# Kernel optimization log

Measured on AMD Instinct MI355X. Metric: run time of the kernel, lower is better.

## Reference

```python
import jax, jax.numpy as jnp
import numpy as np

KS = 5          # B-spline kernel_size per pseudo-coordinate dim
DIM = 2         # pseudo-coordinate dimensionality
NUM_GRAPHS = 64


def spline_conv(x, src, dst, edge_attr, W, root, bias):
    """Degree-1 open B-spline conv (torch-spline-conv semantics, aggr='mean').
    x: [N,Cin], edge_attr: [E,DIM] in [0,1], W: [KS**DIM,Cin,Cout]."""
    N = x.shape[0]
    E = src.shape[0]
    v = edge_attr * (KS - 1)                                   # [E,DIM]
    k_lo = jnp.clip(jnp.floor(v), 0, KS - 2).astype(jnp.int32) # lower knot index
    frac = v - k_lo.astype(v.dtype)                            # [E,DIM]
    # Precompute x @ W_k for all K kernel weights per node: [N,K,Cout]
    xW = jnp.einsum('nc,kco->nko', x, W)
    msg = jnp.zeros((E, W.shape[2]), x.dtype)
    # 2^DIM = 4 nonzero basis products for degree-1 splines
    for bits in ((0, 0), (0, 1), (1, 0), (1, 1)):
        b = jnp.ones((E,), x.dtype)
        wi = jnp.zeros((E,), jnp.int32)
        stride = 1
        for d, bit in enumerate(bits):
            b = b * (frac[:, d] if bit else (1.0 - frac[:, d]))
            wi = wi + (k_lo[:, d] + bit) * stride
            stride *= KS
        msg = msg + b[:, None] * xW[src, wi]                   # gather [E,Cout]
    agg = jax.ops.segment_sum(msg, dst, num_segments=N)
    deg = jax.ops.segment_sum(jnp.ones((E,), x.dtype), dst, num_segments=N)
    agg = agg / jnp.maximum(deg, 1.0)[:, None]                 # mean aggregation
    return agg + x @ root + bias


def setup_inputs() -> dict:
    key = jax.random.key(0)
    ks = jax.random.split(key, 12)
    N, E = 20000, 320000
    Cin, H, O = 1, 32, 10
    K = KS * KS
    p = lambda k, s: jax.random.normal(k, s, jnp.float32) * 0.1
    return {
        'x': jax.random.normal(ks[0], (N, Cin), jnp.float32),
        'edge_attr': jax.random.uniform(ks[1], (E, DIM), jnp.float32),
        'W1': p(ks[2], (K, Cin, H)), 'root1': p(ks[3], (Cin, H)), 'b1': jnp.zeros((H,), jnp.float32),
        'W2': p(ks[4], (K, H, 2 * H)), 'root2': p(ks[5], (H, 2 * H)), 'b2': jnp.zeros((2 * H,), jnp.float32),
        'Wf1': p(ks[6], (2 * H, 128)), 'bf1': jnp.zeros((128,), jnp.float32),
        'Wf2': p(ks[7], (128, O)), 'bf2': jnp.zeros((O,), jnp.float32),
        'edge_index': jax.random.randint(ks[8], (2, E), 0, N),
        'batch': jnp.sort(jax.random.randint(ks[9], (N,), 0, NUM_GRAPHS)),
    }


def reference(x, edge_attr, W1, root1, b1, W2, root2, b2, Wf1, bf1, Wf2, bf2, edge_index, batch):
    src, dst = edge_index[0], edge_index[1]
    h = jax.nn.relu(spline_conv(x, src, dst, edge_attr, W1, root1, b1))
    h = jax.nn.relu(spline_conv(h, src, dst, edge_attr, W2, root2, b2))
    # global mean pool over graphs
    gsum = jax.ops.segment_sum(h, batch, num_segments=NUM_GRAPHS)
    cnt = jax.ops.segment_sum(jnp.ones((h.shape[0],), h.dtype), batch, num_segments=NUM_GRAPHS)
    g = gsum / jnp.maximum(cnt, 1.0)[:, None]
    g = jax.nn.relu(g @ Wf1 + bf1)
    return jax.nn.log_softmax(g @ Wf2 + bf2, axis=1)
```

## Files before the change

kernel.cpp:

```cpp
#include <hip/hip_runtime.h>
#include <hip/hip_fp16.h>
#include <math.h>

#define KK 25
#define H1C 32
#define H2C 64
#define FCC 128
#define NCLS 10
#define NG 64
#define M1 16
#define M2 8

typedef _Float16 v8h __attribute__((ext_vector_type(8)));
typedef _Float16 v4h __attribute__((ext_vector_type(4)));
typedef float v4f __attribute__((ext_vector_type(4)));

__global__ __launch_bounds__(256) void deg_kernel(
    const int* __restrict__ edge_index, int E,
    int* __restrict__ degi,
    const float* __restrict__ W2, __half* __restrict__ W2t) {
    int i = blockIdx.x * 256 + threadIdx.x;
    if (i < KK * H2C * H1C) {
        int c = i & 31, o = (i >> 5) & 63, k = i >> 11;
        W2t[i] = __float2half(W2[(k * H1C + c) * H2C + o]);
    }
    if (i < E) atomicAdd(&degi[edge_index[E + i]], 1);
}

__global__ void scan1_kernel(const int* __restrict__ degi, int N,
                             int* __restrict__ incl, int* __restrict__ bsum) {
    __shared__ int s[256];
    int tid = threadIdx.x;
    int i = blockIdx.x * 256 + tid;
    int v = (i < N) ? degi[i] : 0;
    s[tid] = v;
    __syncthreads();
    for (int off = 1; off < 256; off <<= 1) {
        int t = (tid >= off) ? s[tid - off] : 0;
        __syncthreads();
        s[tid] += t;
        __syncthreads();
    }
    if (i < N) incl[i] = s[tid];
    if (tid == 255) bsum[blockIdx.x] = s[255];
}

__global__ void scan2_kernel(int* __restrict__ bsum, int nb) {
    __shared__ int s[256];
    int tid = threadIdx.x;
    int v = (tid < nb) ? bsum[tid] : 0;
    s[tid] = v;
    __syncthreads();
    for (int off = 1; off < 256; off <<= 1) {
        int t = (tid >= off) ? s[tid - off] : 0;
        __syncthreads();
        s[tid] += t;
        __syncthreads();
    }
    if (tid < nb) bsum[tid] = s[tid] - v;
}

__global__ void scan3_kernel(const int* __restrict__ incl, const int* __restrict__ degi,
                             const int* __restrict__ bsum, int N,
                             int* __restrict__ rowst, int* __restrict__ cur) {
    int i = blockIdx.x * 256 + threadIdx.x;
    if (i >= N) return;
    int r = incl[i] - degi[i] + bsum[blockIdx.x];
    rowst[i] = r;
    cur[i] = r;
}

__global__ void bucket_kernel(const float* __restrict__ edge_attr,
                              const int* __restrict__ edge_index, int E,
                              int* __restrict__ cur, int4* __restrict__ es) {
    int e = blockIdx.x * blockDim.x + threadIdx.x;
    if (e >= E) return;
    float v0 = edge_attr[2 * e + 0] * 4.0f;
    float v1 = edge_attr[2 * e + 1] * 4.0f;
    int k0 = (int)floorf(v0); k0 = min(max(k0, 0), 3);
    int k1 = (int)floorf(v1); k1 = min(max(k1, 0), 3);
    float f0 = v0 - (float)k0, f1 = v1 - (float)k1;
    int dst = edge_index[E + e];
    int pos = atomicAdd(&cur[dst], 1);
    es[pos] = make_int4(edge_index[e], (dst << 8) | (k0 + 5 * k1),
                        __float_as_int(f0), __float_as_int(f1));
}

__global__ __launch_bounds__(256) void l1_kernel(
    const float* __restrict__ x,
    const int* __restrict__ rowst, const int* __restrict__ degi,
    const int4* __restrict__ es,
    const float* __restrict__ W1, const float* __restrict__ root1,
    const float* __restrict__ b1,
    const __half* __restrict__ W2t,
    int N, int E,
    float* __restrict__ h1, __half* __restrict__ xph) {
    __shared__ float w1s[KK * H1C];
    __shared__ float agg1[M1 * H1C];
    __shared__ int4 eb[8][32];
    __shared__ float xb[8][32];
    __shared__ __half h1s[M1][H1C];
    int tid = threadIdx.x;
    for (int i = tid; i < KK * H1C; i += 256) w1s[i] = W1[i];
    for (int i = tid; i < M1 * H1C; i += 256) agg1[i] = 0.0f;
    __syncthreads();
    int g = tid >> 5, o = tid & 31;
    int n0 = blockIdx.x * M1;
    int blkBeg = rowst[n0];
    int blkEnd = (n0 + M1 < N) ? rowst[n0 + M1] : E;
    int total = blkEnd - blkBeg;
    int per = (total + 7) >> 3;
    int wBeg = blkBeg + g * per;
    int wEnd = min(blkEnd, wBeg + per);
    int curDst = -1;
    float acc = 0.0f;
    for (int base = wBeg; base < wEnd; base += 32) {
        int m = min(32, wEnd - base);
        if (o < m) {
            int4 ed = es[base + o];
            eb[g][o] = ed;
            xb[g][o] = x[ed.x];
        }
        for (int j = 0; j < m; j++) {
            int4 ed = eb[g][j];
            float xs = xb[g][j];
            int dst = ed.y >> 8;
            if (dst != curDst) {
                if (curDst >= 0) atomicAdd(&agg1[(curDst - n0) * H1C + o], acc);
                acc = 0.0f;
                curDst = dst;
            }
            float f0 = __int_as_float(ed.z), f1 = __int_as_float(ed.w);
            float g0 = 1.0f - f0, g1 = 1.0f - f1;
            int kb = (ed.y & 0xff) << 5;
            float coef = g0 * g1 * w1s[kb + o] + f0 * g1 * w1s[kb + 32 + o] +
                         g0 * f1 * w1s[kb + 160 + o] + f0 * f1 * w1s[kb + 192 + o];
            acc = fmaf(xs, coef, acc);
        }
    }
    if (curDst >= 0) atomicAdd(&agg1[(curDst - n0) * H1C + o], acc);
    __syncthreads();
#pragma unroll
    for (int i = 0; i < 2; i++) {
        int ln = g + 8 * i;
        int n = n0 + ln;
        if (n < N) {
            float rdeg = 1.0f / fmaxf((float)degi[n], 1.0f);
            float hv = fmaxf(agg1[ln * H1C + o] * rdeg + x[n] * root1[o] + b1[o], 0.0f);
            h1[n * H1C + o] = hv;
            h1s[ln][o] = __float2half(hv);
        } else {
            h1s[ln][o] = __float2half(0.0f);
        }
    }
    __syncthreads();

    int w = tid >> 6, lane = tid & 63;
    int r15 = lane & 15, quad = lane >> 4;
    int o0 = w * 16;
    int bn = n0 + r15;
    bool wr = bn < N;
    v8h bfrag = *(const v8h*)(&h1s[r15][quad * 8]);
    size_t baseoff = (size_t)bn * (KK * H2C) + o0 + (quad << 2);
    for (int k = 0; k < KK; k++) {
        v8h afrag = *(const v8h*)(W2t + ((k << 6) + o0 + r15) * H1C + quad * 8);
        v4f acc2 = {};
        acc2 = __builtin_amdgcn_mfma_f32_16x16x32_f16(afrag, bfrag, acc2, 0, 0, 0);
        if (wr) {
            v4h hv;
            hv[0] = (_Float16)acc2[0];
            hv[1] = (_Float16)acc2[1];
            hv[2] = (_Float16)acc2[2];
            hv[3] = (_Float16)acc2[3];
            *(v4h*)(xph + baseoff + (k << 6)) = hv;
        }
    }
}

__global__ __launch_bounds__(256) void l2_kernel(
    const float* __restrict__ h1,
    const int* __restrict__ rowst, const int* __restrict__ degi,
    const int4* __restrict__ es,
    const unsigned* __restrict__ xphu,
    const float* __restrict__ root2, const float* __restrict__ b2,
    const int* __restrict__ batch,
    int N, int E, float* __restrict__ gsum) {
    __shared__ float agg[M2 * H2C];
    __shared__ int4 eb[4][64];
    int tid = threadIdx.x;
    for (int i = tid; i < M2 * H2C; i += 256) agg[i] = 0.0f;
    __syncthreads();
    int w = tid >> 6, lane = tid & 63;
    int o2 = lane & 31, eh = lane >> 5;
    int n0 = blockIdx.x * M2;
    int blkBeg = rowst[n0];
    int blkEnd = (n0 + M2 < N) ? rowst[n0 + M2] : E;
    int total = blkEnd - blkBeg;
    int per = (total + 3) >> 2;
    int wBeg = blkBeg + w * per;
    int wEnd = min(blkEnd, wBeg + per);
    int curDst = -1;
    float ax = 0.0f, ay = 0.0f;
    for (int base = wBeg; base < wEnd; base += 64) {
        int m = min(64, wEnd - base);
        if (lane < m) eb[w][lane] = es[base + lane];
        for (int j = 0; j < m; j += 2) {
            int jj = j + eh;
            bool act = jj < m;
            int4 ed = eb[w][act ? jj : j];
            const unsigned* p = xphu + (size_t)ed.x * (KK * H2C / 2) +
                                ((ed.y & 0xff) << 5) + o2;
            unsigned t0 = p[0], t1 = p[32], t2 = p[160], t3 = p[192];
            if (act) {
                int dst = ed.y >> 8;
                if (dst != curDst) {
                    if (curDst >= 0) {
                        atomicAdd(&agg[(curDst - n0) * H2C + 2 * o2], ax);
                        atomicAdd(&agg[(curDst - n0) * H2C + 2 * o2 + 1], ay);
                    }
                    ax = ay = 0.0f;
                    curDst = dst;
                }
                float f0 = __int_as_float(ed.z), f1 = __int_as_float(ed.w);
                float g0 = 1.0f - f0, g1 = 1.0f - f1;
                float b0 = g0 * g1, b1 = f0 * g1, bb2 = g0 * f1, b3 = f0 * f1;
                __half2 h0 = *(__half2*)&t0, h1v = *(__half2*)&t1;
                __half2 h2 = *(__half2*)&t2, h3 = *(__half2*)&t3;
                ax = fmaf(b0, __low2float(h0), ax);  ay = fmaf(b0, __high2float(h0), ay);
                ax = fmaf(b1, __low2float(h1v), ax); ay = fmaf(b1, __high2float(h1v), ay);
                ax = fmaf(bb2, __low2float(h2), ax); ay = fmaf(bb2, __high2float(h2), ay);
                ax = fmaf(b3, __low2float(h3), ax);  ay = fmaf(b3, __high2float(h3), ay);
            }
        }
    }
    if (curDst >= 0) {
        atomicAdd(&agg[(curDst - n0) * H2C + 2 * o2], ax);
        atomicAdd(&agg[(curDst - n0) * H2C + 2 * o2 + 1], ay);
    }
    __syncthreads();

#pragma unroll
    for (int i = 0; i < 2; i++) {
        int ln = w + 4 * i;
        int n = n0 + ln;
        if (n < N) {
            float rd = 1.0f / fmaxf((float)degi[n], 1.0f);
            float v = agg[ln * H2C + lane] * rd + b2[lane];
            const float* hr = h1 + n * H1C;
#pragma unroll 8
            for (int c = 0; c < H1C; c++) v = fmaf(hr[c], root2[c * H2C + lane], v);
            agg[ln * H2C + lane] = fmaxf(v, 0.0f);
        } else {
            agg[ln * H2C + lane] = 0.0f;
        }
    }
    __syncthreads();

    if (tid < H2C) {
        float run = 0.0f;
        int curg = batch[n0];
        for (int ln = 0; ln < M2; ln++) {
            int n = n0 + ln;
            if (n >= N) break;
            int gg = batch[n];
            if (gg != curg) {
                atomicAdd(&gsum[curg * H2C + tid], run);
                run = 0.0f;
                curg = gg;
            }
            run += agg[ln * H2C + tid];
        }
        atomicAdd(&gsum[curg * H2C + tid], run);
    }
}

__global__ void head_kernel(const float* __restrict__ gsum,
                            const int* __restrict__ batch, int N,
                            const float* __restrict__ Wf1, const float* __restrict__ bf1,
                            const float* __restrict__ Wf2, const float* __restrict__ bf2,
                            float* __restrict__ out) {
    __shared__ float gc[H2C];
    __shared__ float t1[FCC];
    __shared__ float lg[NCLS];
    __shared__ float lse;
    __shared__ float scnt;
    int g = blockIdx.x, tid = threadIdx.x;
    if (tid == 0) {
        int lo = 0, hi = N;
        while (lo < hi) { int m = (lo + hi) >> 1; if (batch[m] < g) lo = m + 1; else hi = m; }
        int lb = lo;
        lo = 0; hi = N;
        while (lo < hi) { int m = (lo + hi) >> 1; if (batch[m] <= g) lo = m + 1; else hi = m; }
        scnt = (float)(lo - lb);
    }
    __syncthreads();
    if (tid < H2C) gc[tid] = gsum[g * H2C + tid] / fmaxf(scnt, 1.0f);
    __syncthreads();
    {
        float acc = bf1[tid];
        for (int c = 0; c < H2C; c++) acc += gc[c] * Wf1[c * FCC + tid];
        t1[tid] = fmaxf(acc, 0.0f);
    }
    __syncthreads();
    if (tid < NCLS) {
        float acc = bf2[tid];
        for (int j = 0; j < FCC; j++) acc += t1[j] * Wf2[j * NCLS + tid];
        lg[tid] = acc;
    }
    __syncthreads();
    if (tid == 0) {
        float m = lg[0];
        for (int c = 1; c < NCLS; c++) m = fmaxf(m, lg[c]);
        float s = 0.0f;
        for (int c = 0; c < NCLS; c++) s += expf(lg[c] - m);
        lse = m + logf(s);
    }
    __syncthreads();
    if (tid < NCLS) out[g * NCLS + tid] = lg[tid] - lse;
}

extern "C" void kernel_launch(void* const* d_in, const int* in_sizes, int n_in,
                              void* d_out, int out_size, void* d_ws, size_t ws_size,
                              hipStream_t stream) {
    const float* x          = (const float*)d_in[0];
    const float* edge_attr  = (const float*)d_in[1];
    const float* W1         = (const float*)d_in[2];
    const float* root1      = (const float*)d_in[3];
    const float* b1         = (const float*)d_in[4];
    const float* W2         = (const float*)d_in[5];
    const float* root2      = (const float*)d_in[6];
    const float* b2         = (const float*)d_in[7];
    const float* Wf1        = (const float*)d_in[8];
    const float* bf1        = (const float*)d_in[9];
    const float* Wf2        = (const float*)d_in[10];
    const float* bf2        = (const float*)d_in[11];
    const int*   edge_index = (const int*)d_in[12];
    const int*   batch      = (const int*)d_in[13];
    float* out = (float*)d_out;

    const int N = in_sizes[13];
    const int E = in_sizes[12] / 2;
    const int NB = (N + 255) / 256;

    int4*     es   = (int4*)d_ws;
    unsigned* xphu = (unsigned*)(es + E);
    __half*   w2t  = (__half*)(xphu + (size_t)N * 800);
    float* gsum  = (float*)(w2t + KK * H2C * H1C);
    int*   degi  = (int*)(gsum + NG * H2C);
    int*   rowst = degi + N;
    int*   cur   = rowst + N;
    int*   incl  = cur + N;
    int*   bsum  = incl + N;
    float* h1    = (float*)(bsum + 256);

    hipMemsetAsync(gsum, 0, (size_t)NG * H2C * sizeof(float) + (size_t)N * sizeof(int),
                   stream);

    int degBlocks = (E + 255) / 256;
    deg_kernel<<<degBlocks, 256, 0, stream>>>(edge_index, E, degi, W2, w2t);

    scan1_kernel<<<NB, 256, 0, stream>>>(degi, N, incl, bsum);
    scan2_kernel<<<1, 256, 0, stream>>>(bsum, NB);
    scan3_kernel<<<NB, 256, 0, stream>>>(incl, degi, bsum, N, rowst, cur);

    bucket_kernel<<<(E + 255) / 256, 256, 0, stream>>>(edge_attr, edge_index, E, cur, es);

    l1_kernel<<<(N + M1 - 1) / M1, 256, 0, stream>>>(
        x, rowst, degi, es, W1, root1, b1, w2t, N, E, h1, (__half*)xphu);

    l2_kernel<<<(N + M2 - 1) / M2, 256, 0, stream>>>(
        h1, rowst, degi, es, xphu, root2, b2, batch, N, E, gsum);

    head_kernel<<<NG, FCC, 0, stream>>>(gsum, batch, N, Wf1, bf1, Wf2, bf2, out);
}
```

Before: 207.6 us.

## Tile xW layout per 16-node block with LDS-staged coalesced stores; merge scan kernels

Changes the layout of the per-node xW buffer to 16-node tiles ordered [k][node-in-tile][channel], staging MFMA outputs through shared memory so each block writes contiguous 128-byte rows. The layer-2 gather addressing is updated to match. It also merges the second and third scan kernels into one, where each block recomputes its prefix from the block sums, removing a launch. The cost is extra LDS traffic and barriers in l1, and gathers in l2 now span a tile with different locality.

```diff
diff --git a/kernel.cpp b/kernel.cpp
--- a/kernel.cpp
+++ b/kernel.cpp
@@ -10,6 +10,7 @@
 #define NG 64
 #define M1 16
 #define M2 8
+#define TILEU 12800
 
 typedef _Float16 v8h __attribute__((ext_vector_type(8)));
 typedef _Float16 v4h __attribute__((ext_vector_type(4)));
@@ -45,10 +46,14 @@
     if (tid == 255) bsum[blockIdx.x] = s[255];
 }
 
-__global__ void scan2_kernel(int* __restrict__ bsum, int nb) {
+__global__ void scan23_kernel(const int* __restrict__ incl, const int* __restrict__ degi,
+                              const int* __restrict__ bsum, int nb, int N,
+                              int* __restrict__ rowst, int* __restrict__ cur) {
     __shared__ int s[256];
     int tid = threadIdx.x;
-    int v = (tid < nb) ? bsum[tid] : 0;
+    int lim = min(nb, (int)blockIdx.x);
+    int v = 0;
+    for (int j = tid; j < lim; j += 256) v += bsum[j];
     s[tid] = v;
     __syncthreads();
     for (int off = 1; off < 256; off <<= 1) {
@@ -57,17 +62,13 @@
         s[tid] += t;
         __syncthreads();
     }
-    if (tid < nb) bsum[tid] = s[tid] - v;
-}
-
-__global__ void scan3_kernel(const int* __restrict__ incl, const int* __restrict__ degi,
-                             const int* __restrict__ bsum, int N,
-                             int* __restrict__ rowst, int* __restrict__ cur) {
-    int i = blockIdx.x * 256 + threadIdx.x;
-    if (i >= N) return;
-    int r = incl[i] - degi[i] + bsum[blockIdx.x];
-    rowst[i] = r;
-    cur[i] = r;
+    int prior = s[255];
+    int i = blockIdx.x * 256 + tid;
+    if (i < N) {
+        int r = incl[i] - degi[i] + prior;
+        rowst[i] = r;
+        cur[i] = r;
+    }
 }
 
 __global__ void bucket_kernel(const float* __restrict__ edge_attr,
@@ -100,6 +101,7 @@
     __shared__ int4 eb[8][32];
     __shared__ float xb[8][32];
     __shared__ __half h1s[M1][H1C];
+    __shared__ __half stg[5][M1][68];
     int tid = threadIdx.x;
     for (int i = tid; i < KK * H1C; i += 256) w1s[i] = W1[i];
     for (int i = tid; i < M1 * H1C; i += 256) agg1[i] = 0.0f;
@@ -158,22 +160,33 @@
     int w = tid >> 6, lane = tid & 63;
     int r15 = lane & 15, quad = lane >> 4;
     int o0 = w * 16;
-    int bn = n0 + r15;
-    bool wr = bn < N;
     v8h bfrag = *(const v8h*)(&h1s[r15][quad * 8]);
-    size_t baseoff = (size_t)bn * (KK * H2C) + o0 + (quad << 2);
-    for (int k = 0; k < KK; k++) {
-        v8h afrag = *(const v8h*)(W2t + ((k << 6) + o0 + r15) * H1C + quad * 8);
-        v4f acc2 = {};
-        acc2 = __builtin_amdgcn_mfma_f32_16x16x32_f16(afrag, bfrag, acc2, 0, 0, 0);
-        if (wr) {
+    __half* xtile = xph + (size_t)blockIdx.x * (2 * TILEU);
+    int cln = tid >> 4, coc = (tid & 15) * 4;
+    bool crow = (n0 + cln) < N;
+    for (int kc = 0; kc < KK; kc += 5) {
+#pragma unroll
+        for (int kk = 0; kk < 5; kk++) {
+            int k = kc + kk;
+            v8h afrag = *(const v8h*)(W2t + ((k << 6) + o0 + r15) * H1C + quad * 8);
+            v4f acc2 = {};
+            acc2 = __builtin_amdgcn_mfma_f32_16x16x32_f16(afrag, bfrag, acc2, 0, 0, 0);
             v4h hv;
             hv[0] = (_Float16)acc2[0];
             hv[1] = (_Float16)acc2[1];
             hv[2] = (_Float16)acc2[2];
             hv[3] = (_Float16)acc2[3];
-            *(v4h*)(xph + baseoff + (k << 6)) = hv;
-        }
+            *(v4h*)(&stg[kk][r15][o0 + quad * 4]) = hv;
+        }
+        __syncthreads();
+#pragma unroll
+        for (int kk = 0; kk < 5; kk++) {
+            if (crow) {
+                v4h hv = *(const v4h*)(&stg[kk][cln][coc]);
+                *(v4h*)(xtile + ((kc + kk) << 10) + (tid << 2)) = hv;
+            }
+        }
+        __syncthreads();
     }
 }
 
@@ -208,9 +221,9 @@
             int jj = j + eh;
             bool act = jj < m;
             int4 ed = eb[w][act ? jj : j];
-            const unsigned* p = xphu + (size_t)ed.x * (KK * H2C / 2) +
-                                ((ed.y & 0xff) << 5) + o2;
-            unsigned t0 = p[0], t1 = p[32], t2 = p[160], t3 = p[192];
+            const unsigned* p = xphu + (size_t)(ed.x >> 4) * TILEU +
+                                ((ed.y & 0xff) << 9) + ((ed.x & 15) << 5) + o2;
+            unsigned t0 = p[0], t1 = p[512], t2 = p[2560], t3 = p[3072];
             if (act) {
                 int dst = ed.y >> 8;
                 if (dst != curDst) {
@@ -341,10 +354,11 @@
     const int N = in_sizes[13];
     const int E = in_sizes[12] / 2;
     const int NB = (N + 255) / 256;
+    const int NT1 = (N + M1 - 1) / M1;
 
     int4*     es   = (int4*)d_ws;
     unsigned* xphu = (unsigned*)(es + E);
-    __half*   w2t  = (__half*)(xphu + (size_t)N * 800);
+    __half*   w2t  = (__half*)(xphu + (size_t)NT1 * TILEU);
     float* gsum  = (float*)(w2t + KK * H2C * H1C);
     int*   degi  = (int*)(gsum + NG * H2C);
     int*   rowst = degi + N;
@@ -360,12 +374,11 @@
     deg_kernel<<<degBlocks, 256, 0, stream>>>(edge_index, E, degi, W2, w2t);
 
     scan1_kernel<<<NB, 256, 0, stream>>>(degi, N, incl, bsum);
-    scan2_kernel<<<1, 256, 0, stream>>>(bsum, NB);
-    scan3_kernel<<<NB, 256, 0, stream>>>(incl, degi, bsum, N, rowst, cur);
+    scan23_kernel<<<NB, 256, 0, stream>>>(incl, degi, bsum, NB, N, rowst, cur);
 
     bucket_kernel<<<(E + 255) / 256, 256, 0, stream>>>(edge_attr, edge_index, E, cur, es);
 
-    l1_kernel<<<(N + M1 - 1) / M1, 256, 0, stream>>>(
+    l1_kernel<<<NT1, 256, 0, stream>>>(
         x, rowst, degi, es, W1, root1, b1, w2t, N, E, h1, (__half*)xphu);
 
     l2_kernel<<<(N + M2 - 1) / M2, 256, 0, stream>>>(
```

Measured after the change: 198.5 us. 4.4% less time.
